# Optimization experiments

Measured on AMD Instinct MI355X. Metric: run time of the kernel, lower is better.

Reference implementation:

```python
import jax, jax.numpy as jnp
import numpy as np

B, TY, ENC, EMB, DEC, V = 16, 255, 512, 256, 512, 32000
EPS = 1e-5


def _lstm(x, Wih, Whh, bih, bhh):
    # x: [B, T, Din]; torch gate order i, f, g, o; h0 = c0 = 0
    Bb = x.shape[0]
    H = Whh.shape[1]
    xw = jnp.einsum('btd,gd->btg', x, Wih) + bih + bhh  # [B, T, 4H]

    def step(carry, xt):
        h, c = carry
        g = xt + h @ Whh.T
        i, f, gg, o = jnp.split(g, 4, axis=-1)
        i = jax.nn.sigmoid(i)
        f = jax.nn.sigmoid(f)
        gg = jnp.tanh(gg)
        o = jax.nn.sigmoid(o)
        c = f * c + i * gg
        h = o * jnp.tanh(c)
        return (h, c), h

    h0 = jnp.zeros((Bb, H), x.dtype)
    _, hs = jax.lax.scan(step, (h0, h0), jnp.swapaxes(xw, 0, 1))
    return jnp.swapaxes(hs, 0, 1)  # [B, T, H]


def setup_inputs():
    key = jax.random.key(0)
    ks = jax.random.split(key, 16)
    s = 0.05
    rn = lambda k, sh: jax.random.normal(k, sh, jnp.float32)
    return {
        'x': rn(ks[0], (B, ENC)),
        'y': jax.random.randint(ks[1], (B, TY), 0, V),
        'fc1_w': rn(ks[2], (EMB, ENC)) * s,
        'fc1_b': rn(ks[3], (EMB,)) * s,
        'bn_g': jnp.ones((EMB,), jnp.float32),
        'bn_b': jnp.zeros((EMB,), jnp.float32),
        'emb': rn(ks[4], (V, EMB)) * s,
        'l1_Wih': rn(ks[5], (4 * DEC, EMB)) * s,
        'l1_Whh': rn(ks[6], (4 * DEC, DEC)) * s,
        'l1_bih': rn(ks[7], (4 * DEC,)) * s,
        'l1_bhh': rn(ks[8], (4 * DEC,)) * s,
        'attn_Wout': rn(ks[9], (DEC, 2 * DEC)) * s,
        'dc_Wih': rn(ks[10], (4 * DEC, DEC)) * s,
        'dc_Whh': rn(ks[11], (4 * DEC, DEC)) * s,
        'dc_bih': rn(ks[12], (4 * DEC,)) * s,
        'dc_bhh': rn(ks[13], (4 * DEC,)) * s,
        'fc2_w': rn(ks[14], (V, DEC)) * s,
        'fc2_b': rn(ks[15], (V,)) * s,
        'lengths': TY + 1,  # all sequences full length
    }


def reference(x, y, fc1_w, fc1_b, bn_g, bn_b, emb, l1_Wih, l1_Whh, l1_bih, l1_bhh,
              attn_Wout, dc_Wih, dc_Whh, dc_bih, dc_bhh, fc2_w, fc2_b, lengths):
    # fc1 + BatchNorm1d (training-mode batch stats, biased var)
    feat = x @ fc1_w.T + fc1_b                         # [B, EMB]
    mu = feat.mean(axis=0)
    var = feat.var(axis=0)
    feat = (feat - mu) / jnp.sqrt(var + EPS) * bn_g + bn_b
    # prepend feature to embedded tokens -> [B, L, EMB], L = TY + 1
    seq = jnp.concatenate([feat[:, None, :], emb[y]], axis=1)
    # first LSTM
    h = _lstm(seq, l1_Wih, l1_Whh, l1_bih, l1_bhh)     # [B, L, DEC]
    L = seq.shape[1]
    # causal dot-product self-attention (vectorized form of the python loop)
    scores = jnp.einsum('bqd,bkd->bqk', h, h)
    mask = jnp.tril(jnp.ones((L, L), bool))
    w = jax.nn.softmax(jnp.where(mask, scores, -1e30), axis=-1)
    mix = jnp.einsum('bqk,bkd->bqd', w, h)
    attn = jnp.tanh(jnp.concatenate([mix, h], axis=-1) @ attn_Wout.T)
    # decoder LSTM cell over attended features
    out = _lstm(attn, dc_Wih, dc_Whh, dc_bih, dc_bhh)  # [B, L, DEC]
    return out @ fc2_w.T + fc2_b                       # [B, L, V]
```

## Files before the change

kernel.cpp:

```cpp
#include <hip/hip_runtime.h>

#define BB 16
#define TY 255
#define ENC 512
#define EMBD 256
#define DEC 512
#define VV 32000
#define LL 256
#define M4 4096
#define GG 2048
#define SENT 0x7FC0

typedef unsigned short u16;
typedef __attribute__((ext_vector_type(8))) short short8;
typedef __attribute__((ext_vector_type(4))) float f32x4;
typedef __attribute__((ext_vector_type(4))) unsigned short u16x4;

__device__ __forceinline__ u16 f2bf(float f) {
  unsigned u = __float_as_uint(f);
  u += 0x7fff + ((u >> 16) & 1);
  return (u16)(u >> 16);
}
__device__ __forceinline__ f32x4 mfma16(short8 a, short8 b, f32x4 c) {
  return __builtin_amdgcn_mfma_f32_16x16x32_bf16(a, b, c, 0, 0, 0);
}
__device__ __forceinline__ float sigmoidf_(float x) { return 1.f / (1.f + expf(-x)); }

__device__ __forceinline__ void st_b32_dev(int* a, int v) {
  asm volatile("global_store_dword %0, %1, off sc1" :: "v"(a), "v"(v) : "memory");
}

template<bool BT, bool OBF, bool DOTANH, bool BIAS>
__global__ __launch_bounds__(256) void gemm_kernel(
    const u16* __restrict__ A, const u16* __restrict__ Bm, void* __restrict__ Cv,
    const float* __restrict__ bias,
    int K, int lda, int ldb, int ldc,
    long a_bs, long b_bs, long c_bs)
{
  __shared__ u16 As[64][72];
  __shared__ u16 Bs[64][72];
  const int tid = threadIdx.x;
  const long m0 = (long)blockIdx.y * 64, n0 = (long)blockIdx.x * 64;
  const int z = blockIdx.z;
  const u16* Ab = A + (long)z * a_bs;
  const u16* Bb = Bm + (long)z * b_bs;
  const int lane = tid & 63, w = tid >> 6;
  const int wm = w >> 1, wn = w & 1;
  f32x4 acc[2][2] = {};
  for (int k0 = 0; k0 < K; k0 += 64) {
#pragma unroll
    for (int i = 0; i < 2; i++) {
      int c = tid + 256 * i;
      int r = c >> 3, kk = (c & 7) << 3;
      *(short8*)&As[r][kk] = *(const short8*)&Ab[(m0 + r) * (long)lda + k0 + kk];
    }
    if (BT) {
#pragma unroll
      for (int i = 0; i < 2; i++) {
        int c = tid + 256 * i;
        int r = c >> 3, kk = (c & 7) << 3;
        *(short8*)&Bs[r][kk] = *(const short8*)&Bb[(n0 + r) * (long)ldb + k0 + kk];
      }
    } else {
#pragma unroll
      for (int i = 0; i < 2; i++) {
        int c = tid + 256 * i;
        int kk = c >> 3, nn = (c & 7) << 3;
        const u16* s = &Bb[(long)(k0 + kk) * ldb + n0 + nn];
#pragma unroll
        for (int j = 0; j < 8; j++) Bs[nn + j][kk] = s[j];
      }
    }
    __syncthreads();
#pragma unroll
    for (int kf = 0; kf < 2; kf++) {
      const int ko = kf * 32 + (lane >> 4) * 8;
      short8 a0 = *(const short8*)&As[wm * 32 + (lane & 15)][ko];
      short8 a1 = *(const short8*)&As[wm * 32 + 16 + (lane & 15)][ko];
      short8 b0 = *(const short8*)&Bs[wn * 32 + (lane & 15)][ko];
      short8 b1 = *(const short8*)&Bs[wn * 32 + 16 + (lane & 15)][ko];
      acc[0][0] = mfma16(a0, b0, acc[0][0]);
      acc[0][1] = mfma16(a0, b1, acc[0][1]);
      acc[1][0] = mfma16(a1, b0, acc[1][0]);
      acc[1][1] = mfma16(a1, b1, acc[1][1]);
    }
    __syncthreads();
  }
#pragma unroll
  for (int m = 0; m < 2; m++)
#pragma unroll
    for (int n = 0; n < 2; n++) {
#pragma unroll
      for (int r = 0; r < 4; r++) {
        long row = m0 + wm * 32 + m * 16 + (lane >> 4) * 4 + r;
        long col = n0 + wn * 32 + n * 16 + (lane & 15);
        float v = acc[m][n][r];
        if (BIAS) v += bias[col];
        if (DOTANH) v = tanhf(v);
        if (OBF) ((u16*)Cv)[(long)z * c_bs + row * ldc + col] = f2bf(v);
        else ((float*)Cv)[(long)z * c_bs + row * ldc + col] = v;
      }
    }
}

__global__ void sentinel_kernel(u16* __restrict__ p) {
  long i = ((long)blockIdx.x * 256 + threadIdx.x) * 8;
  short v = (i < 8192) ? (short)0 : (short)SENT;
  short8 s = {v, v, v, v, v, v, v, v};
  *(short8*)&p[i] = s;
}

template<int MODE>
__global__ __launch_bounds__(256) void lstm_kernel(
    const float* __restrict__ xw,
    const u16* __restrict__ Whh,
    u16* __restrict__ Hseq,
    u16* __restrict__ hout)
{
  const int nb = blockIdx.x;
  const int tid = threadIdx.x;
  const int lane = tid & 63, w = tid >> 6;
  __shared__ u16 hs[16][520];
  __shared__ float gbuf[16][64];
  const int ncol0 = nb * 64 + w * 16;
  short8 bfrag[16];
  {
    const u16* wr = Whh + (long)(ncol0 + (lane & 15)) * 512 + ((lane >> 4) * 8);
#pragma unroll
    for (int kf = 0; kf < 16; kf++) bfrag[kf] = *(const short8*)&wr[kf * 32];
  }
  const int b = tid >> 4, jl = tid & 15;
  const int jglob = nb * 16 + jl;
  int cc[4];
#pragma unroll
  for (int i = 0; i < 4; i++) cc[i] = (tid + i * 256 + nb * 32) & 1023;
  float c = 0.f;
  float4 xg = *(const float4*)&xw[((long)b * LL) * GG + nb * 64 + jl * 4];
  for (int t = 0; t < LL; t++) {
    const u16* Hin = Hseq + (long)t * 8192;
    short8 sv[4];
    int bad;
    do {
#pragma unroll
      for (int i = 0; i < 4; i++)
        asm volatile("global_load_dwordx4 %0, %1, off sc1"
                     : "=v"(sv[i]) : "v"(Hin + (cc[i] >> 6) * 512 + (cc[i] & 63) * 8));
      asm volatile("s_waitcnt vmcnt(0)" ::: "memory");
      __builtin_amdgcn_sched_barrier(0);
      bad = 0;
#pragma unroll
      for (int i = 0; i < 4; i++) {
        const int* dv = (const int*)&sv[i];
#pragma unroll
        for (int d = 0; d < 4; d++) bad |= ((dv[d] & 0xFFFF) == SENT);
      }
    } while (__any(bad != 0));
    __builtin_amdgcn_sched_barrier(0);
#pragma unroll
    for (int i = 0; i < 4; i++)
      *(short8*)&hs[cc[i] >> 6][(cc[i] & 63) * 8] = sv[i];
    __syncthreads();
    f32x4 acc0 = {}, acc1 = {};
#pragma unroll
    for (int kf = 0; kf < 8; kf++) {
      short8 a0 = *(const short8*)&hs[lane & 15][(lane >> 4) * 8 + (2 * kf) * 32];
      short8 a1 = *(const short8*)&hs[lane & 15][(lane >> 4) * 8 + (2 * kf + 1) * 32];
      acc0 = mfma16(a0, bfrag[2 * kf], acc0);
      acc1 = mfma16(a1, bfrag[2 * kf + 1], acc1);
    }
    f32x4 acc = acc0 + acc1;
#pragma unroll
    for (int r = 0; r < 4; r++)
      gbuf[(lane >> 4) * 4 + r][w * 16 + (lane & 15)] = acc[r];
    __syncthreads();
    float gi = sigmoidf_(gbuf[b][jl * 4 + 0] + xg.x);
    float gf = sigmoidf_(gbuf[b][jl * 4 + 1] + xg.y);
    float gg = tanhf(gbuf[b][jl * 4 + 2] + xg.z);
    float go = sigmoidf_(gbuf[b][jl * 4 + 3] + xg.w);
    c = gf * c + gi * gg;
    float h = go * tanhf(c);
    u16 hb = f2bf(h);
    unsigned hi16 = (unsigned)__shfl_down((int)(unsigned)hb, 1);
    if ((jl & 1) == 0) {
      int pk = (int)((unsigned)hb | (hi16 << 16));
      st_b32_dev((int*)&Hseq[((long)t + 1) * 8192 + b * 512 + jglob], pk);
    }
    if (MODE == 0) hout[((long)b * LL + t) * 1024 + 512 + jglob] = hb;
    else           hout[((long)b * LL + t) * 512 + jglob] = hb;
    if (t + 1 < LL)
      xg = *(const float4*)&xw[((long)b * LL + (t + 1)) * GG + nb * 64 + jl * 4];
  }
}

__global__ void fc1_kernel(const float* __restrict__ x, const float* __restrict__ wgt,
                           const float* __restrict__ bias, float* __restrict__ feat) {
  __shared__ float xs[ENC];
  int bb = blockIdx.x, j = threadIdx.x;
  for (int k = j; k < ENC; k += 256) xs[k] = x[bb * ENC + k];
  __syncthreads();
  float s = bias[j];
  const float* wr = wgt + (long)j * ENC;
  for (int k = 0; k < ENC; k += 4) {
    float4 wv = *(const float4*)&wr[k];
    s += xs[k] * wv.x + xs[k + 1] * wv.y + xs[k + 2] * wv.z + xs[k + 3] * wv.w;
  }
  feat[bb * EMBD + j] = s;
}

__global__ void bn_embed0_kernel(const float* __restrict__ feat, const float* __restrict__ g,
                                 const float* __restrict__ bb, u16* __restrict__ seq) {
  int j = threadIdx.x;
  float mu = 0.f, m2 = 0.f;
  for (int i = 0; i < BB; i++) { float v = feat[i * EMBD + j]; mu += v; m2 += v * v; }
  mu *= (1.f / BB);
  float var = m2 * (1.f / BB) - mu * mu;
  float sc = g[j] * rsqrtf(var + 1e-5f);
  float sh = bb[j];
  for (int i = 0; i < BB; i++) {
    float v = (feat[i * EMBD + j] - mu) * sc + sh;
    seq[((long)i * LL) * EMBD + j] = f2bf(v);
  }
}

__global__ void embed_kernel(const int* __restrict__ y, const float* __restrict__ emb,
                             u16* __restrict__ seq) {
  int t = blockIdx.x, bb = blockIdx.y;
  int tok = y[bb * TY + t];
  int j = threadIdx.x;
  seq[((long)bb * LL + 1 + t) * EMBD + j] = f2bf(emb[(long)tok * EMBD + j]);
}

__global__ __launch_bounds__(256) void softmax_kernel(const float* __restrict__ sc,
                                                      u16* __restrict__ wsm) {
  int row = blockIdx.x;
  int q = row & (LL - 1);
  int k = threadIdx.x;
  __shared__ float red[8];
  float v = (k <= q) ? sc[(long)row * LL + k] : -3.4e38f;
  float m = v;
#pragma unroll
  for (int o = 32; o > 0; o >>= 1) m = fmaxf(m, __shfl_xor(m, o));
  if ((k & 63) == 0) red[k >> 6] = m;
  __syncthreads();
  m = fmaxf(fmaxf(red[0], red[1]), fmaxf(red[2], red[3]));
  float e = (k <= q) ? expf(v - m) : 0.f;
  float s = e;
#pragma unroll
  for (int o = 32; o > 0; o >>= 1) s += __shfl_xor(s, o);
  if ((k & 63) == 0) red[4 + (k >> 6)] = s;
  __syncthreads();
  s = red[4] + red[5] + red[6] + red[7];
  wsm[(long)row * LL + k] = f2bf(e / s);
}

__global__ void conv_bf16_kernel(const float* __restrict__ s, u16* __restrict__ d) {
  long i = ((long)blockIdx.x * 256 + threadIdx.x) * 4;
  float4 v = *(const float4*)&s[i];
  u16x4 o = {f2bf(v.x), f2bf(v.y), f2bf(v.z), f2bf(v.w)};
  *(u16x4*)&d[i] = o;
}

__global__ void conv_lstm_w_kernel(const float* __restrict__ s, u16* __restrict__ d, int ldk) {
  int n = blockIdx.x;
  int r = (n & 3) * DEC + (n >> 2);
  for (int k = threadIdx.x; k < ldk; k += 256)
    d[(long)n * ldk + k] = f2bf(s[(long)r * ldk + k]);
}

__global__ void conv_lstm_b_kernel(const float* __restrict__ bih, const float* __restrict__ bhh,
                                   float* __restrict__ d) {
  int n = blockIdx.x * 256 + threadIdx.x;
  int r = (n & 3) * DEC + (n >> 2);
  d[n] = bih[r] + bhh[r];
}

extern "C" void kernel_launch(void* const* d_in, const int* in_sizes, int n_in,
                              void* d_out, int out_size, void* d_ws, size_t ws_size,
                              hipStream_t stream) {
  const float* x      = (const float*)d_in[0];
  const int*   y      = (const int*)d_in[1];
  const float* fc1_w  = (const float*)d_in[2];
  const float* fc1_b  = (const float*)d_in[3];
  const float* bn_g   = (const float*)d_in[4];
  const float* bn_b   = (const float*)d_in[5];
  const float* emb    = (const float*)d_in[6];
  const float* l1_Wih = (const float*)d_in[7];
  const float* l1_Whh = (const float*)d_in[8];
  const float* l1_bih = (const float*)d_in[9];
  const float* l1_bhh = (const float*)d_in[10];
  const float* Wout   = (const float*)d_in[11];
  const float* dc_Wih = (const float*)d_in[12];
  const float* dc_Whh = (const float*)d_in[13];
  const float* dc_bih = (const float*)d_in[14];
  const float* dc_bhh = (const float*)d_in[15];
  const float* fc2_w  = (const float*)d_in[16];
  const float* fc2_b  = (const float*)d_in[17];
  float* out = (float*)d_out;

  char* ws = (char*)d_ws;
  float* xw     = (float*)(ws + 0);
  u16*   seqb   = (u16*)(ws + 33554432);
  u16*   cat    = (u16*)(ws + 35651584);
  float* scores = (float*)(ws + 44040192);
  u16*   Hseq   = (u16*)(ws + 44040192);
  u16*   wsm    = (u16*)(ws + 48234496);
  u16*   attnb  = (u16*)(ws + 50331648);
  u16*   h2b    = (u16*)(ws + 54525952);
  u16*   wih1   = (u16*)(ws + 58720256);
  u16*   whh1   = (u16*)(ws + 59768832);
  u16*   wih2   = (u16*)(ws + 61865984);
  u16*   whh2   = (u16*)(ws + 63963136);
  u16*   woutb  = (u16*)(ws + 66060288);
  u16*   fc2wb  = (u16*)(ws + 67108864);
  float* b1p    = (float*)(ws + 99876864);
  float* b2p    = (float*)(ws + 99885056);
  float* feat   = (float*)(ws + 99893248);

  conv_lstm_w_kernel<<<GG, 256, 0, stream>>>(l1_Wih, wih1, EMBD);
  conv_lstm_w_kernel<<<GG, 256, 0, stream>>>(l1_Whh, whh1, DEC);
  conv_lstm_w_kernel<<<GG, 256, 0, stream>>>(dc_Wih, wih2, DEC);
  conv_lstm_w_kernel<<<GG, 256, 0, stream>>>(dc_Whh, whh2, DEC);
  conv_lstm_b_kernel<<<GG / 256, 256, 0, stream>>>(l1_bih, l1_bhh, b1p);
  conv_lstm_b_kernel<<<GG / 256, 256, 0, stream>>>(dc_bih, dc_bhh, b2p);
  conv_bf16_kernel<<<(DEC * 2 * DEC) / 1024, 256, 0, stream>>>(Wout, woutb);
  conv_bf16_kernel<<<(VV * DEC) / 1024, 256, 0, stream>>>(fc2_w, fc2wb);

  fc1_kernel<<<BB, 256, 0, stream>>>(x, fc1_w, fc1_b, feat);
  bn_embed0_kernel<<<1, 256, 0, stream>>>(feat, bn_g, bn_b, seqb);
  embed_kernel<<<dim3(TY, BB), 256, 0, stream>>>(y, emb, seqb);

  gemm_kernel<true, false, false, true><<<dim3(GG / 64, M4 / 64, 1), 256, 0, stream>>>(
      seqb, wih1, xw, b1p, EMBD, EMBD, EMBD, GG, 0, 0, 0);
  sentinel_kernel<<<1028, 256, 0, stream>>>(Hseq);
  lstm_kernel<0><<<32, 256, 0, stream>>>(xw, whh1, Hseq, cat);
  gemm_kernel<true, false, false, false><<<dim3(LL / 64, LL / 64, BB), 256, 0, stream>>>(
      cat + 512, cat + 512, scores, nullptr, DEC, 1024, 1024, LL,
      (long)LL * 1024, (long)LL * 1024, (long)LL * LL);
  softmax_kernel<<<M4, 256, 0, stream>>>(scores, wsm);
  gemm_kernel<false, true, false, false><<<dim3(DEC / 64, LL / 64, BB), 256, 0, stream>>>(
      wsm, cat + 512, cat, nullptr, LL, LL, 1024, 1024,
      (long)LL * LL, (long)LL * 1024, (long)LL * 1024);
  gemm_kernel<true, true, true, false><<<dim3(DEC / 64, M4 / 64, 1), 256, 0, stream>>>(
      cat, woutb, attnb, nullptr, 1024, 1024, 1024, DEC, 0, 0, 0);
  gemm_kernel<true, false, false, true><<<dim3(GG / 64, M4 / 64, 1), 256, 0, stream>>>(
      attnb, wih2, xw, b2p, DEC, DEC, DEC, GG, 0, 0, 0);
  sentinel_kernel<<<1028, 256, 0, stream>>>(Hseq);
  lstm_kernel<1><<<32, 256, 0, stream>>>(xw, whh2, Hseq, h2b);
  gemm_kernel<true, false, false, true><<<dim3(VV / 64, M4 / 64, 1), 256, 0, stream>>>(
      h2b, fc2wb, out, fc2_b, DEC, DEC, DEC, VV, 0, 0, 0);
}
```

Before: 1.580 ms.

## Add 128x128-tile GEMM kernel with direct global-to-LDS loads

Adds a new bf16 MFMA GEMM kernel that computes 128x128 output tiles per block, with each wave owning a 64x64 sub-tile and a 64-wide K step. Operand tiles are copied with the global_load_lds builtin, so data goes from global memory straight into LDS without passing through registers. The kernel replaces the old 64x64 kernel for all B-transposed GEMMs, including the large vocabulary projection. The aim is more data reuse per LDS load, fewer blocks, and less load overhead. In exchange, the unpadded LDS layout may cause bank conflicts, more accumulator registers are needed, and small GEMMs now launch fewer blocks.

```diff
diff --git a/kernel.cpp b/kernel.cpp
--- a/kernel.cpp
+++ b/kernel.cpp
@@ -28,6 +28,11 @@
 
 __device__ __forceinline__ void st_b32_dev(int* a, int v) {
   asm volatile("global_store_dword %0, %1, off sc1" :: "v"(a), "v"(v) : "memory");
+}
+__device__ __forceinline__ void gload_lds16(const u16* g, u16* l) {
+  __builtin_amdgcn_global_load_lds(
+      (const __attribute__((address_space(1))) void*)g,
+      (__attribute__((address_space(3))) void*)l, 16, 0, 0);
 }
 
 template<bool BT, bool OBF, bool DOTANH, bool BIAS>
@@ -95,6 +100,68 @@
         long row = m0 + wm * 32 + m * 16 + (lane >> 4) * 4 + r;
         long col = n0 + wn * 32 + n * 16 + (lane & 15);
         float v = acc[m][n][r];
+        if (BIAS) v += bias[col];
+        if (DOTANH) v = tanhf(v);
+        if (OBF) ((u16*)Cv)[(long)z * c_bs + row * ldc + col] = f2bf(v);
+        else ((float*)Cv)[(long)z * c_bs + row * ldc + col] = v;
+      }
+    }
+}
+
+template<bool OBF, bool DOTANH, bool BIAS>
+__global__ __launch_bounds__(256) void gemm128_kernel(
+    const u16* __restrict__ A, const u16* __restrict__ Bm, void* __restrict__ Cv,
+    const float* __restrict__ bias,
+    int K, int lda, int ldb, int ldc,
+    long a_bs, long b_bs, long c_bs)
+{
+  __shared__ u16 As[128 * 64];
+  __shared__ u16 Bs[128 * 64];
+  const int tid = threadIdx.x;
+  const long m0 = (long)blockIdx.y * 128, n0 = (long)blockIdx.x * 128;
+  const int z = blockIdx.z;
+  const u16* Ab = A + (long)z * a_bs;
+  const u16* Bb = Bm + (long)z * b_bs;
+  const int lane = tid & 63, w = tid >> 6;
+  const int wm = w >> 1, wn = w & 1;
+  const int rr = tid >> 3, kk = (tid & 7) << 3;
+  f32x4 acc[4][4] = {};
+  for (int k0 = 0; k0 < K; k0 += 64) {
+#pragma unroll
+    for (int i = 0; i < 4; i++) {
+      gload_lds16(&Ab[(m0 + i * 32 + rr) * (long)lda + k0 + kk],
+                  As + (i * 256 + (w << 6)) * 8);
+      gload_lds16(&Bb[(n0 + i * 32 + rr) * (long)ldb + k0 + kk],
+                  Bs + (i * 256 + (w << 6)) * 8);
+    }
+    __syncthreads();
+#pragma unroll
+    for (int kf = 0; kf < 2; kf++) {
+      const int ko = kf * 32 + (lane >> 4) * 8;
+      short8 a[4], b[4];
+#pragma unroll
+      for (int mi = 0; mi < 4; mi++)
+        a[mi] = *(const short8*)&As[(wm * 64 + mi * 16 + (lane & 15)) * 64 + ko];
+#pragma unroll
+      for (int ni = 0; ni < 4; ni++)
+        b[ni] = *(const short8*)&Bs[(wn * 64 + ni * 16 + (lane & 15)) * 64 + ko];
+#pragma unroll
+      for (int mi = 0; mi < 4; mi++)
+#pragma unroll
+        for (int ni = 0; ni < 4; ni++)
+          acc[mi][ni] = mfma16(a[mi], b[ni], acc[mi][ni]);
+    }
+    __syncthreads();
+  }
+#pragma unroll
+  for (int mi = 0; mi < 4; mi++)
+#pragma unroll
+    for (int ni = 0; ni < 4; ni++) {
+#pragma unroll
+      for (int r = 0; r < 4; r++) {
+        long row = m0 + wm * 64 + mi * 16 + (lane >> 4) * 4 + r;
+        long col = n0 + wn * 64 + ni * 16 + (lane & 15);
+        float v = acc[mi][ni][r];
         if (BIAS) v += bias[col];
         if (DOTANH) v = tanhf(v);
         if (OBF) ((u16*)Cv)[(long)z * c_bs + row * ldc + col] = f2bf(v);
@@ -329,23 +396,23 @@
   bn_embed0_kernel<<<1, 256, 0, stream>>>(feat, bn_g, bn_b, seqb);
   embed_kernel<<<dim3(TY, BB), 256, 0, stream>>>(y, emb, seqb);
 
-  gemm_kernel<true, false, false, true><<<dim3(GG / 64, M4 / 64, 1), 256, 0, stream>>>(
+  gemm128_kernel<false, false, true><<<dim3(GG / 128, M4 / 128, 1), 256, 0, stream>>>(
       seqb, wih1, xw, b1p, EMBD, EMBD, EMBD, GG, 0, 0, 0);
   sentinel_kernel<<<1028, 256, 0, stream>>>(Hseq);
   lstm_kernel<0><<<32, 256, 0, stream>>>(xw, whh1, Hseq, cat);
-  gemm_kernel<true, false, false, false><<<dim3(LL / 64, LL / 64, BB), 256, 0, stream>>>(
+  gemm128_kernel<false, false, false><<<dim3(LL / 128, LL / 128, BB), 256, 0, stream>>>(
       cat + 512, cat + 512, scores, nullptr, DEC, 1024, 1024, LL,
       (long)LL * 1024, (long)LL * 1024, (long)LL * LL);
   softmax_kernel<<<M4, 256, 0, stream>>>(scores, wsm);
   gemm_kernel<false, true, false, false><<<dim3(DEC / 64, LL / 64, BB), 256, 0, stream>>>(
       wsm, cat + 512, cat, nullptr, LL, LL, 1024, 1024,
       (long)LL * LL, (long)LL * 1024, (long)LL * 1024);
-  gemm_kernel<true, true, true, false><<<dim3(DEC / 64, M4 / 64, 1), 256, 0, stream>>>(
+  gemm128_kernel<true, true, false><<<dim3(DEC / 128, M4 / 128, 1), 256, 0, stream>>>(
       cat, woutb, attnb, nullptr, 1024, 1024, 1024, DEC, 0, 0, 0);
-  gemm_kernel<true, false, false, true><<<dim3(GG / 64, M4 / 64, 1), 256, 0, stream>>>(
+  gemm128_kernel<false, false, true><<<dim3(GG / 128, M4 / 128, 1), 256, 0, stream>>>(
       attnb, wih2, xw, b2p, DEC, DEC, DEC, GG, 0, 0, 0);
   sentinel_kernel<<<1028, 256, 0, stream>>>(Hseq);
   lstm_kernel<1><<<32, 256, 0, stream>>>(xw, whh2, Hseq, h2b);
-  gemm_kernel<true, false, false, true><<<dim3(VV / 64, M4 / 64, 1), 256, 0, stream>>>(
+  gemm128_kernel<false, false, true><<<dim3(VV / 128, M4 / 128, 1), 256, 0, stream>>>(
       h2b, fc2wb, out, fc2_b, DEC, DEC, DEC, VV, 0, 0, 0);
 }
```

Result: faster. 1.466 ms (-7.2%).
